# Performance work log

Measured on AMD Instinct MI355X. Metric: run time of the kernel, lower is better.

The kernel has to match this reference:

```python
import jax, jax.numpy as jnp
import numpy as np
from jax import lax

K = 4
OUT_PLANES = 128
TEMPERATURE = 30.0


def setup_inputs() -> dict:
    key = jax.random.key(0)
    ks = jax.random.split(key, 5)
    in_planes, k = 128, 3
    he_std = float(np.sqrt(2.0)) * (in_planes * k * k) ** (-0.5)
    return {
        "x": jax.random.normal(ks[0], (16, in_planes, 64, 64), jnp.float32),
        "weight": jax.random.normal(ks[1], (K * OUT_PLANES, in_planes, k, k), jnp.float32) * he_std,
        "bias": jax.random.normal(ks[2], (K * OUT_PLANES,), jnp.float32) * 0.01,
        "se_w1": jax.random.normal(ks[3], (33, in_planes), jnp.float32) * (2.0 / 33) ** 0.5,
        "se_w2": jax.random.normal(ks[4], (K, 33), jnp.float32) * (2.0 / K) ** 0.5,
        "se_b2": jnp.zeros((K,), jnp.float32),
    }


def reference(x, weight, bias, se_w1, se_w2, se_b2):
    B = x.shape[0]
    # SE attention: global avg pool -> fc1 -> relu -> fc2 -> softmax(./T)
    pooled = x.mean(axis=(2, 3))                      # [B, Cin]
    h = jax.nn.relu(pooled @ se_w1.T)                 # [B, hidden]
    logits = h @ se_w2.T + se_b2                      # [B, K]
    attn = jax.nn.softmax(logits / TEMPERATURE, axis=1)
    # conv with K*out channels (groups=1, stride=1, pad=1, dil=1)
    y = lax.conv_general_dilated(
        x, weight, window_strides=(1, 1), padding=[(1, 1), (1, 1)],
        dimension_numbers=("NCHW", "OIHW", "NCHW"))
    y = y + bias[None, :, None, None]                 # [B, K*out, Ho, Wo]
    Ho, Wo = y.shape[2], y.shape[3]
    y = y.reshape(B, K, OUT_PLANES, Ho, Wo)
    # attention-weighted combine over K branches (bmm in torch)
    return jnp.einsum("bk,bkohw->bohw", attn, y)
```

## Files before the change

kernel.cpp:

```cpp
#include <hip/hip_runtime.h>
#include <cstdint>
#include <cstddef>

typedef unsigned short u16;
typedef __attribute__((ext_vector_type(8))) short short8;
typedef __attribute__((ext_vector_type(4))) float f32x4;

__device__ __forceinline__ u16 f2bf(float f){
  union { float f; unsigned u; } c; c.f = f;
  unsigned u = c.u;
  u += 0x7fffu + ((u >> 16) & 1u);
  return (u16)(u >> 16);
}
__device__ __forceinline__ unsigned pk2(float a, float b){
  union { float f; unsigned u; } ca, cb; ca.f = a; cb.f = b;
  return ((ca.u + 0x8000u) >> 16) | ((cb.u + 0x8000u) & 0xFFFF0000u);
}

#define XB_STRIDE 557568
#define XR_STRIDE 8448


#define GLD_LDS(gsrc, ldst) \
  __builtin_amdgcn_global_load_lds((const __attribute__((address_space(1))) void*)(gsrc), \
                                   (__attribute__((address_space(3))) void*)(ldst), 16, 0, 0)

__global__ __launch_bounds__(256) void xpose_pool(
    const float* __restrict__ x, u16* __restrict__ xT2, float* __restrict__ part)
{
  const int bid = blockIdx.x;
  const int b = bid & 15, chunk = bid >> 4;
  const int pos0 = chunk << 7;
  const int tid = threadIdx.x;
  __shared__ u16 tile[16384];
  __shared__ float psum[128 * 33];
  const float* xb = x + ((size_t)b << 19) + pos0;
  const int p4 = (tid & 31) << 2;
  const int swz = (tid & 31) & 7;

  if (chunk == 0){
    u16* xh = xT2 + (size_t)b * XB_STRIDE;
    for (int i = tid; i < 4160; i += 256){
      const int p = i >> 4, oct = i & 15;
      int row, col;
      if (p < 66)      { row = 0;        col = p; }
      else if (p < 132){ row = 65;       col = p - 66; }
      else if (p < 196){ row = p - 131;  col = 0; }
      else             { row = p - 195;  col = 65; }
      *(uint4*)(xh + row * XR_STRIDE + (col << 7) + (oct << 3)) =
          make_uint4(0u, 0u, 0u, 0u);
    }
  }

  #pragma unroll
  for (int i = 0; i < 2; ++i){
    const int gci = (tid >> 5) + (i << 3);
    const int ci8 = gci << 3;
    float4 L[8];
    #pragma unroll
    for (int j = 0; j < 8; ++j)
      L[j] = *(const float4*)(xb + ((size_t)(ci8 + j) << 12) + p4);
    #pragma unroll
    for (int j = 0; j < 8; ++j)
      psum[(ci8 + j) * 33 + (tid & 31)] = L[j].x + L[j].y + L[j].z + L[j].w;
    const int gs = gci ^ swz;
    const float* e = (const float*)L;
    #pragma unroll
    for (int p = 0; p < 4; ++p){
      const int row = p4 + p;
      uint4 V;
      V.x = pk2(e[0 * 4 + p], e[1 * 4 + p]);
      V.y = pk2(e[2 * 4 + p], e[3 * 4 + p]);
      V.z = pk2(e[4 * 4 + p], e[5 * 4 + p]);
      V.w = pk2(e[6 * 4 + p], e[7 * 4 + p]);
      *(uint4*)(tile + (row << 7) + (gs << 3)) = V;
    }
  }
  __syncthreads();

  if (tid < 128){
    float s = 0.f;
    #pragma unroll 8
    for (int j = 0; j < 32; ++j) s += psum[tid * 33 + j];
    part[((b << 5) + chunk) * 128 + tid] = s;
  }

  u16* xo = xT2 + (size_t)b * XB_STRIDE;
  const int g = tid & 15, rb = (tid >> 4) << 3;
  #pragma unroll
  for (int r = 0; r < 8; ++r){
    const int row = rb + r;
    const int gs = g ^ ((row >> 2) & 7);
    uint4 v = *(const uint4*)(tile + (row << 7) + (gs << 3));
    const int pos = pos0 + row;
    const int h = pos >> 6, w = pos & 63;
    *(uint4*)(xo + (h + 1) * XR_STRIDE + ((w + 1) << 7) + (g << 3)) = v;
  }
}

__global__ void attn_fc(const float* __restrict__ part, const float* __restrict__ w1,
                        const float* __restrict__ w2, const float* __restrict__ b2,
                        float* __restrict__ attn)
{
  const int b = blockIdx.x, t = threadIdx.x;
  __shared__ float sp[128];
  __shared__ float sh[33];
  __shared__ float sl[4];
  const float* pb = part + (b << 12);
  float s = 0.f;
  for (int c = 0; c < 32; ++c) s += pb[(c << 7) + t];
  sp[t] = s * (1.f / 4096.f);
  __syncthreads();
  if (t < 33){
    float h = 0.f;
    for (int ci = 0; ci < 128; ++ci) h += sp[ci] * w1[t * 128 + ci];
    sh[t] = fmaxf(h, 0.f);
  }
  __syncthreads();
  if (t < 4){
    float l = b2[t];
    for (int j = 0; j < 33; ++j) l += sh[j] * w2[t * 33 + j];
    sl[t] = l * (1.f / 30.f);
  }
  __syncthreads();
  if (t == 0){
    float m = fmaxf(fmaxf(sl[0], sl[1]), fmaxf(sl[2], sl[3]));
    float e0 = __expf(sl[0] - m), e1 = __expf(sl[1] - m);
    float e2 = __expf(sl[2] - m), e3 = __expf(sl[3] - m);
    float inv = 1.f / (e0 + e1 + e2 + e3);
    attn[(b << 2) + 0] = e0 * inv; attn[(b << 2) + 1] = e1 * inv;
    attn[(b << 2) + 2] = e2 * inv; attn[(b << 2) + 3] = e3 * inv;
  }
}

__global__ __launch_bounds__(256) void combine(
    const float* __restrict__ W, const float* __restrict__ bias,
    const float* __restrict__ attn, u16* __restrict__ wcomb,
    float* __restrict__ bcomb)
{
  __shared__ float wlds[9216];
  const int bid = blockIdx.x;
  const int b = bid & 15, cp = bid >> 4;
  const int tid = threadIdx.x;
  const float a0 = attn[(b << 2) + 0], a1 = attn[(b << 2) + 1];
  const float a2 = attn[(b << 2) + 2], a3 = attn[(b << 2) + 3];

  #pragma unroll
  for (int it = 0; it < 9; ++it){
    const int G = it * 256 + tid;
    const int k = G / 576, rem = G - k * 576;
    const int co_l = rem / 288, j4 = rem - co_l * 288;
    const float* src = W + (size_t)(k * 128 + (cp << 1) + co_l) * 1152 + (j4 << 2);
    GLD_LDS(src, (char*)wlds + (G << 4));
  }

  if (tid < 2){
    const int co = (cp << 1) + tid;
    bcomb[(b << 7) + co] = a0 * bias[co] + a1 * bias[128 + co]
                         + a2 * bias[256 + co] + a3 * bias[384 + co];
  }
  asm volatile("s_waitcnt vmcnt(0)" ::: "memory");
  __syncthreads();

  u16* wob = wcomb + (size_t)b * 147456;
  for (int gi = tid; gi < 288; gi += 256){
    const int co_l = gi / 144;
    const int r = gi - co_l * 144;
    const int tap = r >> 4;
    const int gg = r & 15;
    const int cq = gg >> 2, g = gg & 3;
    const int co = (cp << 1) + co_l;
    union { u16 h[8]; uint4 v; } pk;
    #pragma unroll
    for (int e = 0; e < 8; ++e){
      const int ci = (cq << 5) + (g << 3) + e;
      const int j = ci * 9 + tap;
      float s = a0 * wlds[co_l * 1152 + j]        + a1 * wlds[2304 + co_l * 1152 + j]
              + a2 * wlds[4608 + co_l * 1152 + j] + a3 * wlds[6912 + co_l * 1152 + j];
      pk.h[e] = f2bf(s);
    }
    *(uint4*)(wob + (((tap << 2) + cq) << 12) + (co << 5) + (g << 3)) = pk.v;
  }
}

__global__ __launch_bounds__(256, 2) void conv_mfma(
    const u16* __restrict__ xT2, const u16* __restrict__ wcomb,
    const float* __restrict__ bcomb, float* __restrict__ out)
{
  extern __shared__ char smem[];
  u16* s_x = (u16*)smem;
  u16* s_w = (u16*)(smem + 16896);

  const int tid = threadIdx.x;
  const int lane = tid & 63, wid = tid >> 6;
  const int wr = wid & 1, wcv = wid >> 1;
  const int l15 = lane & 15, hi = lane >> 4;

  const int bid = blockIdx.x;
  const int b = bid & 15;
  const int h0 = (bid >> 4) << 1;

  const u16* Abase = wcomb + (size_t)b * 147456;
  const u16* Xbase = xT2 + (size_t)b * XB_STRIDE;

#define STAGE_X(Q) { \
    _Pragma("unroll") \
    for (int _it = 0; _it < 5; ++_it){ \
      const int _G = _it * 256 + tid; \
      if (_it < 4 || _G < 1056){ \
        const int _oct = _G & 3, _t = _G >> 2; \
        const int _col = _t % 66, _row = _t / 66; \
        const u16* _src = Xbase + (h0 + _row) * XR_STRIDE + (_col << 7) \
                        + ((Q) << 5) + (_oct << 3); \
        GLD_LDS(_src, s_x + (_G << 3)); \
      } \
    } }

#define STAGE_W(Q, TAP, BUF) { \
    const u16* _As = Abase + (((((TAP) << 2) + (Q))) << 12); \
    u16* _sw = s_w + (BUF) * 4096; \
    GLD_LDS(_As + (tid << 3), _sw + (tid << 3)); \
    GLD_LDS(_As + ((tid + 256) << 3), _sw + ((tid + 256) << 3)); }

#define COMPUTE(TAP, BUF) { \
    const int _dh = (TAP) / 3, _dw = (TAP) - 3 * (_dh); \
    const u16* _sw = s_w + (BUF) * 4096; \
    short8 _af[4], _bf[4]; \
    _Pragma("unroll") \
    for (int _a = 0; _a < 4; ++_a){ \
      const int _co = (wcv << 6) + (_a << 4) + l15; \
      _af[_a] = *(const short8*)(_sw + (_co << 5) + (hi << 3)); \
    } \
    _Pragma("unroll") \
    for (int _p = 0; _p < 4; ++_p){ \
      const int _col = l15 + _dw + (_p << 4); \
      _bf[_p] = *(const short8*)(s_x + (((wr + _dh) * 66 + _col) << 5) + (hi << 3)); \
    } \
    _Pragma("unroll") \
    for (int _a = 0; _a < 4; ++_a) \
      _Pragma("unroll") \
      for (int _p = 0; _p < 4; ++_p) \
        acc[_a][_p] = __builtin_amdgcn_mfma_f32_16x16x32_bf16(_af[_a], _bf[_p], acc[_a][_p], 0, 0, 0); }

#define VM0_BAR { asm volatile("s_waitcnt vmcnt(0)" ::: "memory"); __syncthreads(); }

  f32x4 acc[4][4] = {};

  STAGE_X(0);
  STAGE_W(0, 0, 0);
  VM0_BAR;

  int buf = 0;
  for (int q = 0; q < 4; ++q){
    #pragma unroll
    for (int tap = 0; tap < 9; ++tap){
      if (!(q == 3 && tap == 8)){
        const int nq = (tap == 8) ? q + 1 : q;
        const int nt = (tap == 8) ? 0 : tap + 1;
        STAGE_W(nq, nt, buf ^ 1);
      }
      COMPUTE(tap, buf);
      VM0_BAR;
      buf ^= 1;
      if (tap == 8 && q < 3){
        STAGE_X(q + 1);
        VM0_BAR;
      }
    }
  }

#undef VM0_BAR
#undef COMPUTE
#undef STAGE_W
#undef STAGE_X

  const int hrow = h0 + wr;
  float* ob = out + ((size_t)b << 19) + (hrow << 6) + l15;
  #pragma unroll
  for (int a = 0; a < 4; ++a){
    const int co0 = (wcv << 6) + (a << 4) + (hi << 2);
    #pragma unroll
    for (int r = 0; r < 4; ++r){
      const float bc = bcomb[(b << 7) + co0 + r];
      float* op = ob + (size_t)(co0 + r) * 4096;
      #pragma unroll
      for (int p = 0; p < 4; ++p)
        __builtin_nontemporal_store(acc[a][p][r] + bc, op + (p << 4));
    }
  }
}

extern "C" void kernel_launch(void* const* d_in, const int* in_sizes, int n_in,
                              void* d_out, int out_size, void* d_ws, size_t ws_size,
                              hipStream_t stream)
{
  const float* x    = (const float*)d_in[0];
  const float* W    = (const float*)d_in[1];
  const float* bias = (const float*)d_in[2];
  const float* w1   = (const float*)d_in[3];
  const float* w2   = (const float*)d_in[4];
  const float* b2   = (const float*)d_in[5];
  float* out = (float*)d_out;

  char* ws = (char*)d_ws;
  float* part  = (float*)(ws);
  float* attn  = (float*)(ws + 262144);
  float* bcomb = (float*)(ws + 262400);
  u16*   xT2   = (u16*)  (ws + 270592);
  u16*   wcomb = (u16*)  (ws + 18112768);

  xpose_pool<<<512, 256, 0, stream>>>(x, xT2, part);
  attn_fc<<<16, 128, 0, stream>>>(part, w1, w2, b2, attn);
  combine<<<1024, 256, 0, stream>>>(W, bias, attn, wcomb, bcomb);

  (void)hipFuncSetAttribute(reinterpret_cast<const void*>(conv_mfma),
                            hipFuncAttributeMaxDynamicSharedMemorySize, 33280);
  conv_mfma<<<512, 256, 33280, stream>>>(xT2, wcomb, bcomb, out);
}
```

Before: 50.06 us.

## Fuse SE attention into combine kernel and double conv K-chunk per barrier

Removes the separate attn_fc launch by recomputing the SE MLP and softmax inside each combine block, overlapping it with the async weight loads. The conv kernel now stages 64 input channels per X tile and 64-channel weight slices per tap, halving the number of barrier-synchronized stages, and adds an XOR swizzle on the x tile to avoid LDS bank conflicts. In exchange each combine block redundantly computes attention, and the conv kernel's LDS use doubles to about 65 KB, which may limit how many blocks fit per CU.

```diff
diff --git a/kernel.cpp b/kernel.cpp
--- a/kernel.cpp
+++ b/kernel.cpp
@@ -98,52 +98,19 @@
   }
 }
 
-__global__ void attn_fc(const float* __restrict__ part, const float* __restrict__ w1,
-                        const float* __restrict__ w2, const float* __restrict__ b2,
-                        float* __restrict__ attn)
+__global__ __launch_bounds__(256) void combine(
+    const float* __restrict__ W, const float* __restrict__ bias,
+    const float* __restrict__ part, const float* __restrict__ w1,
+    const float* __restrict__ w2, const float* __restrict__ b2,
+    u16* __restrict__ wcomb, float* __restrict__ bcomb)
 {
-  const int b = blockIdx.x, t = threadIdx.x;
+  __shared__ float wlds[9216];
   __shared__ float sp[128];
   __shared__ float sh[33];
-  __shared__ float sl[4];
-  const float* pb = part + (b << 12);
-  float s = 0.f;
-  for (int c = 0; c < 32; ++c) s += pb[(c << 7) + t];
-  sp[t] = s * (1.f / 4096.f);
-  __syncthreads();
-  if (t < 33){
-    float h = 0.f;
-    for (int ci = 0; ci < 128; ++ci) h += sp[ci] * w1[t * 128 + ci];
-    sh[t] = fmaxf(h, 0.f);
-  }
-  __syncthreads();
-  if (t < 4){
-    float l = b2[t];
-    for (int j = 0; j < 33; ++j) l += sh[j] * w2[t * 33 + j];
-    sl[t] = l * (1.f / 30.f);
-  }
-  __syncthreads();
-  if (t == 0){
-    float m = fmaxf(fmaxf(sl[0], sl[1]), fmaxf(sl[2], sl[3]));
-    float e0 = __expf(sl[0] - m), e1 = __expf(sl[1] - m);
-    float e2 = __expf(sl[2] - m), e3 = __expf(sl[3] - m);
-    float inv = 1.f / (e0 + e1 + e2 + e3);
-    attn[(b << 2) + 0] = e0 * inv; attn[(b << 2) + 1] = e1 * inv;
-    attn[(b << 2) + 2] = e2 * inv; attn[(b << 2) + 3] = e3 * inv;
-  }
-}
-
-__global__ __launch_bounds__(256) void combine(
-    const float* __restrict__ W, const float* __restrict__ bias,
-    const float* __restrict__ attn, u16* __restrict__ wcomb,
-    float* __restrict__ bcomb)
-{
-  __shared__ float wlds[9216];
+  __shared__ float sat[4];
   const int bid = blockIdx.x;
   const int b = bid & 15, cp = bid >> 4;
   const int tid = threadIdx.x;
-  const float a0 = attn[(b << 2) + 0], a1 = attn[(b << 2) + 1];
-  const float a2 = attn[(b << 2) + 2], a3 = attn[(b << 2) + 3];
 
   #pragma unroll
   for (int it = 0; it < 9; ++it){
@@ -154,13 +121,43 @@
     GLD_LDS(src, (char*)wlds + (G << 4));
   }
 
+  if (tid < 128){
+    const float* pb = part + (b << 12);
+    float s = 0.f;
+    #pragma unroll 8
+    for (int c = 0; c < 32; ++c) s += pb[(c << 7) + tid];
+    sp[tid] = s * (1.f / 4096.f);
+  }
+  __syncthreads();
+  if (tid < 33){
+    float h = 0.f;
+    for (int ci = 0; ci < 128; ++ci) h += sp[ci] * w1[tid * 128 + ci];
+    sh[tid] = fmaxf(h, 0.f);
+  }
+  __syncthreads();
+  if (tid == 0){
+    float l[4];
+    #pragma unroll
+    for (int t = 0; t < 4; ++t){
+      float v = b2[t];
+      for (int j = 0; j < 33; ++j) v += sh[j] * w2[t * 33 + j];
+      l[t] = v * (1.f / 30.f);
+    }
+    float m = fmaxf(fmaxf(l[0], l[1]), fmaxf(l[2], l[3]));
+    float e0 = __expf(l[0] - m), e1 = __expf(l[1] - m);
+    float e2 = __expf(l[2] - m), e3 = __expf(l[3] - m);
+    float inv = 1.f / (e0 + e1 + e2 + e3);
+    sat[0] = e0 * inv; sat[1] = e1 * inv; sat[2] = e2 * inv; sat[3] = e3 * inv;
+  }
+  asm volatile("s_waitcnt vmcnt(0)" ::: "memory");
+  __syncthreads();
+  const float a0 = sat[0], a1 = sat[1], a2 = sat[2], a3 = sat[3];
+
   if (tid < 2){
     const int co = (cp << 1) + tid;
     bcomb[(b << 7) + co] = a0 * bias[co] + a1 * bias[128 + co]
                          + a2 * bias[256 + co] + a3 * bias[384 + co];
   }
-  asm volatile("s_waitcnt vmcnt(0)" ::: "memory");
-  __syncthreads();
 
   u16* wob = wcomb + (size_t)b * 147456;
   for (int gi = tid; gi < 288; gi += 256){
@@ -189,7 +186,7 @@
 {
   extern __shared__ char smem[];
   u16* s_x = (u16*)smem;
-  u16* s_w = (u16*)(smem + 16896);
+  u16* s_w = (u16*)(smem + 33792);
 
   const int tid = threadIdx.x;
   const int lane = tid & 63, wid = tid >> 6;
@@ -203,44 +200,51 @@
   const u16* Abase = wcomb + (size_t)b * 147456;
   const u16* Xbase = xT2 + (size_t)b * XB_STRIDE;
 
-#define STAGE_X(Q) { \
+#define STAGE_X(HF) { \
     _Pragma("unroll") \
-    for (int _it = 0; _it < 5; ++_it){ \
+    for (int _it = 0; _it < 9; ++_it){ \
       const int _G = _it * 256 + tid; \
-      if (_it < 4 || _G < 1056){ \
-        const int _oct = _G & 3, _t = _G >> 2; \
+      if (_it < 8 || _G < 2112){ \
+        const int _slot = _G & 7, _t = _G >> 3; \
         const int _col = _t % 66, _row = _t / 66; \
         const u16* _src = Xbase + (h0 + _row) * XR_STRIDE + (_col << 7) \
-                        + ((Q) << 5) + (_oct << 3); \
+                        + ((HF) << 6) + ((_slot ^ ((_col & 1) << 2)) << 3); \
         GLD_LDS(_src, s_x + (_G << 3)); \
       } \
     } }
 
-#define STAGE_W(Q, TAP, BUF) { \
-    const u16* _As = Abase + (((((TAP) << 2) + (Q))) << 12); \
-    u16* _sw = s_w + (BUF) * 4096; \
-    GLD_LDS(_As + (tid << 3), _sw + (tid << 3)); \
-    GLD_LDS(_As + ((tid + 256) << 3), _sw + ((tid + 256) << 3)); }
+#define STAGE_W(HF, TAP, BUF) { \
+    const u16* _As = Abase + ((((TAP) << 2) + ((HF) << 1)) << 12); \
+    u16* _sw = s_w + (BUF) * 8192; \
+    _Pragma("unroll") \
+    for (int _it = 0; _it < 4; ++_it){ \
+      const int _G = _it * 256 + tid; \
+      GLD_LDS(_As + (_G << 3), _sw + (_G << 3)); \
+    } }
 
 #define COMPUTE(TAP, BUF) { \
     const int _dh = (TAP) / 3, _dw = (TAP) - 3 * (_dh); \
-    const u16* _sw = s_w + (BUF) * 4096; \
-    short8 _af[4], _bf[4]; \
+    const u16* _sw = s_w + (BUF) * 8192; \
     _Pragma("unroll") \
-    for (int _a = 0; _a < 4; ++_a){ \
-      const int _co = (wcv << 6) + (_a << 4) + l15; \
-      _af[_a] = *(const short8*)(_sw + (_co << 5) + (hi << 3)); \
-    } \
-    _Pragma("unroll") \
-    for (int _p = 0; _p < 4; ++_p){ \
-      const int _col = l15 + _dw + (_p << 4); \
-      _bf[_p] = *(const short8*)(s_x + (((wr + _dh) * 66 + _col) << 5) + (hi << 3)); \
-    } \
-    _Pragma("unroll") \
-    for (int _a = 0; _a < 4; ++_a) \
+    for (int _ks = 0; _ks < 2; ++_ks){ \
+      short8 _af[4], _bf[4]; \
       _Pragma("unroll") \
-      for (int _p = 0; _p < 4; ++_p) \
-        acc[_a][_p] = __builtin_amdgcn_mfma_f32_16x16x32_bf16(_af[_a], _bf[_p], acc[_a][_p], 0, 0, 0); }
+      for (int _a = 0; _a < 4; ++_a){ \
+        const int _co = (wcv << 6) + (_a << 4) + l15; \
+        _af[_a] = *(const short8*)(_sw + (_ks << 12) + (_co << 5) + (hi << 3)); \
+      } \
+      _Pragma("unroll") \
+      for (int _p = 0; _p < 4; ++_p){ \
+        const int _col = l15 + _dw + (_p << 4); \
+        const int _sl = ((_ks << 2) + hi) ^ ((_col & 1) << 2); \
+        _bf[_p] = *(const short8*)(s_x + ((((wr + _dh) * 66 + _col) << 6) + (_sl << 3))); \
+      } \
+      _Pragma("unroll") \
+      for (int _a = 0; _a < 4; ++_a) \
+        _Pragma("unroll") \
+        for (int _p = 0; _p < 4; ++_p) \
+          acc[_a][_p] = __builtin_amdgcn_mfma_f32_16x16x32_bf16(_af[_a], _bf[_p], acc[_a][_p], 0, 0, 0); \
+    } }
 
 #define VM0_BAR { asm volatile("s_waitcnt vmcnt(0)" ::: "memory"); __syncthreads(); }
 
@@ -251,19 +255,19 @@
   VM0_BAR;
 
   int buf = 0;
-  for (int q = 0; q < 4; ++q){
+  for (int hf = 0; hf < 2; ++hf){
     #pragma unroll
     for (int tap = 0; tap < 9; ++tap){
-      if (!(q == 3 && tap == 8)){
-        const int nq = (tap == 8) ? q + 1 : q;
+      if (!(hf == 1 && tap == 8)){
+        const int nh = (tap == 8) ? 1 : hf;
         const int nt = (tap == 8) ? 0 : tap + 1;
-        STAGE_W(nq, nt, buf ^ 1);
+        STAGE_W(nh, nt, buf ^ 1);
       }
       COMPUTE(tap, buf);
       VM0_BAR;
       buf ^= 1;
-      if (tap == 8 && q < 3){
-        STAGE_X(q + 1);
+      if (tap == 8 && hf == 0){
+        STAGE_X(1);
         VM0_BAR;
       }
     }
@@ -304,16 +308,14 @@
 
   char* ws = (char*)d_ws;
   float* part  = (float*)(ws);
-  float* attn  = (float*)(ws + 262144);
-  float* bcomb = (float*)(ws + 262400);
+  float* bcomb = (float*)(ws + 262144);
   u16*   xT2   = (u16*)  (ws + 270592);
   u16*   wcomb = (u16*)  (ws + 18112768);
 
   xpose_pool<<<512, 256, 0, stream>>>(x, xT2, part);
-  attn_fc<<<16, 128, 0, stream>>>(part, w1, w2, b2, attn);
-  combine<<<1024, 256, 0, stream>>>(W, bias, attn, wcomb, bcomb);
+  combine<<<1024, 256, 0, stream>>>(W, bias, part, w1, w2, b2, wcomb, bcomb);
 
   (void)hipFuncSetAttribute(reinterpret_cast<const void*>(conv_mfma),
-                            hipFuncAttributeMaxDynamicSharedMemorySize, 33280);
-  conv_mfma<<<512, 256, 33280, stream>>>(xT2, wcomb, bcomb, out);
-}
+                            hipFuncAttributeMaxDynamicSharedMemorySize, 66560);
+  conv_mfma<<<512, 256, 66560, stream>>>(xT2, wcomb, bcomb, out);
+}
```

Result: no change. 50.33 us (+0.5%).
